# Optimization experiments

Measured on AMD Instinct MI355X. Metric: run time of the kernel, lower is better.

## Reference

```python
import jax, jax.numpy as jnp
import numpy as np

IN_F = 4096
OUT_F = 16384
TOKENS = 64


def setup_inputs() -> dict:
    key = jax.random.key(0)
    k1, k2, k3 = jax.random.split(key, 3)
    x = jax.random.normal(k1, (TOKENS, IN_F), dtype=jnp.float16)
    # int8-valued weights stored as int32 (same math after cast to fp16)
    weight = jax.random.randint(k2, (OUT_F, IN_F), -127, 127, dtype=jnp.int32)
    weight_scales = jax.random.uniform(k3, (OUT_F,), dtype=jnp.float16, minval=0.001, maxval=0.02)
    bias = jnp.zeros((1, OUT_F), dtype=jnp.float16)
    return {"x": x, "weight": weight, "weight_scales": weight_scales, "bias": bias}


def reference(x, weight, weight_scales, bias):
    # Dequantize int8 weight to fp16 with per-output-channel scale, then linear.
    w_fp16 = weight.astype(jnp.float16) * weight_scales[:, None]  # [out, in]
    y = jnp.dot(x, w_fp16.T) + bias  # [tokens, out]
    return y
```

## Files before the change

### kernel.cpp

```cpp
#include <hip/hip_runtime.h>
#include <hip/hip_bf16.h>
#include <hip/hip_fp16.h>

#define IN_F 4096
#define OUT_F 16384
#define TOKENS 64

#define NCH 64
#define KT 64
#define KHALF 2048
#define NTILES (KHALF / KT)
#define BLOCK 256

typedef __attribute__((ext_vector_type(8))) short bf16x8;
typedef __attribute__((ext_vector_type(8))) unsigned short u16x8;
typedef __attribute__((ext_vector_type(4))) unsigned short u16x4;
typedef __attribute__((ext_vector_type(4))) float f32x4;
typedef __attribute__((ext_vector_type(4))) int i32x4;

enum { F_BF16 = 0, F_FP16 = 1, F_FP32 = 2 };

__device__ __forceinline__ float dec_bf16(unsigned short h) {
    return __uint_as_float(((unsigned)h) << 16);
}
__device__ __forceinline__ float dec_fp16(unsigned short h) {
    __half_raw hr; hr.x = h;
    return __half2float(__half(hr));
}
__device__ __forceinline__ unsigned short enc_bf16_rne(float f) {
    unsigned u = __float_as_uint(f);
    u += 0x7FFFu + ((u >> 16) & 1u);
    return (unsigned short)(u >> 16);
}

__device__ __forceinline__ int detect_fmt16(const void* p, int lane, float lo, float hi) {
    unsigned short h = ((const unsigned short*)p)[lane];
    float vb = fabsf(dec_bf16(h));
    float vh = fabsf(dec_fp16(h));
    int cb = __popcll(__ballot(vb > lo && vb < hi));
    int ch = __popcll(__ballot(vh > lo && vh < hi));
    return (cb >= 56) ? F_BF16 : (ch >= 56) ? F_FP16 : F_FP32;
}
__device__ __forceinline__ int detect_wint(const int* w, int lane) {
    int v = w[lane];
    int ci = __popcll(__ballot(v >= -127 && v <= 127));
    return (ci >= 56) ? 1 : 0;
}

__global__ __launch_bounds__(256) void prep_x(const void* __restrict__ xv,
                                              unsigned short* __restrict__ xbf) {
    const int tid  = blockIdx.x * 256 + threadIdx.x;
    const int lane = threadIdx.x & 63;
    const int xf = detect_fmt16(xv, lane, 9.7e-4f, 64.0f);

    if (xf == F_BF16) {
        u16x8 a = ((const u16x8*)xv)[tid * 2];
        u16x8 b = ((const u16x8*)xv)[tid * 2 + 1];
        ((u16x8*)xbf)[tid * 2]     = a;
        ((u16x8*)xbf)[tid * 2 + 1] = b;
    } else if (xf == F_FP32) {
        u16x8 o[2];
        #pragma unroll
        for (int half = 0; half < 2; ++half) {
            f32x4 v0 = ((const f32x4*)xv)[tid * 4 + half * 2];
            f32x4 v1 = ((const f32x4*)xv)[tid * 4 + half * 2 + 1];
            #pragma unroll
            for (int j = 0; j < 4; ++j) {
                o[half][j]     = enc_bf16_rne(v0[j]);
                o[half][j + 4] = enc_bf16_rne(v1[j]);
            }
        }
        ((u16x8*)xbf)[tid * 2]     = o[0];
        ((u16x8*)xbf)[tid * 2 + 1] = o[1];
    } else {
        #pragma unroll
        for (int half = 0; half < 2; ++half) {
            u16x8 v = ((const u16x8*)xv)[tid * 2 + half];
            u16x8 o;
            #pragma unroll
            for (int j = 0; j < 8; ++j) o[j] = enc_bf16_rne(dec_fp16(v[j]));
            ((u16x8*)xbf)[tid * 2 + half] = o;
        }
    }
}

template <int WINT>
__device__ __forceinline__ void tile_compute(const char* __restrict__ bB,
                                             const char* __restrict__ bA,
                                             int wv, int ln, int kq, f32x4 acc[4]) {
    const char* brow = bB + (wv * 16 + ln) * 256;
    #pragma unroll
    for (int s = 0; s < 2; ++s) {
        const int c0 = s * 8 + kq * 2;
        i32x4 b0 = *(const i32x4*)(brow + ((c0)     ^ ln) * 16);
        i32x4 b1 = *(const i32x4*)(brow + ((c0 + 1) ^ ln) * 16);
        bf16x8 bfrag;
        #pragma unroll
        for (int j = 0; j < 4; ++j) {
            unsigned f0 = WINT ? __float_as_uint((float)b0[j]) : (unsigned)b0[j];
            unsigned f1 = WINT ? __float_as_uint((float)b1[j]) : (unsigned)b1[j];
            bfrag[j]     = (short)(f0 >> 16);
            bfrag[j + 4] = (short)(f1 >> 16);
        }
        const int ca = s * 4 + kq;
        bf16x8 a0 = *(const bf16x8*)(bA + (ln      ) * 128 + ((ca) ^ (ln & 7)) * 16);
        bf16x8 a1 = *(const bf16x8*)(bA + (ln + 16) * 128 + ((ca) ^ (ln & 7)) * 16);
        bf16x8 a2 = *(const bf16x8*)(bA + (ln + 32) * 128 + ((ca) ^ (ln & 7)) * 16);
        bf16x8 a3 = *(const bf16x8*)(bA + (ln + 48) * 128 + ((ca) ^ (ln & 7)) * 16);
        acc[0] = __builtin_amdgcn_mfma_f32_16x16x32_bf16(a0, bfrag, acc[0], 0, 0, 0);
        acc[1] = __builtin_amdgcn_mfma_f32_16x16x32_bf16(a1, bfrag, acc[1], 0, 0, 0);
        acc[2] = __builtin_amdgcn_mfma_f32_16x16x32_bf16(a2, bfrag, acc[2], 0, 0, 0);
        acc[3] = __builtin_amdgcn_mfma_f32_16x16x32_bf16(a3, bfrag, acc[3], 0, 0, 0);
    }
}

__global__ __launch_bounds__(BLOCK) void w8a16_main(
    const int* __restrict__ w, const unsigned short* __restrict__ xbf,
    float* __restrict__ pws) {

    __shared__ alignas(16) char ldsB[2][NCH * KT * 4];
    __shared__ alignas(16) char ldsA[2][TOKENS * KT * 2];

    const int tid  = threadIdx.x;
    const int wv   = tid >> 6;
    const int lane = tid & 63;
    const int ln   = lane & 15;
    const int kq   = lane >> 4;

    const int kh   = blockIdx.x & 1;
    const int n0   = (blockIdx.x >> 1) * NCH;
    const int koff = kh * KHALF;

    const int wi = detect_wint(w, lane);

    auto stage = [&](int t, int db) {
        #pragma unroll
        for (int j = 0; j < 4; ++j) {
            const int idx = j * 256 + tid;
            const int r   = idx >> 4;
            const int cg  = (idx & 15) ^ (r & 15);
            const int* g  = w + (size_t)(n0 + r) * IN_F + koff + t * KT + cg * 4;
            __builtin_amdgcn_global_load_lds(
                (const __attribute__((address_space(1))) unsigned int*)g,
                (__attribute__((address_space(3))) unsigned int*)(&ldsB[db][idx * 16]),
                16, 0, 0);
        }
        #pragma unroll
        for (int j = 0; j < 2; ++j) {
            const int idx = j * 256 + tid;
            const int tok = idx >> 3;
            const int cg  = (idx & 7) ^ (tok & 7);
            const unsigned short* g = xbf + (size_t)tok * IN_F + koff + t * KT + cg * 8;
            __builtin_amdgcn_global_load_lds(
                (const __attribute__((address_space(1))) unsigned int*)g,
                (__attribute__((address_space(3))) unsigned int*)(&ldsA[db][idx * 16]),
                16, 0, 0);
        }
    };

    f32x4 acc[4] = {};

    stage(0, 0);
    __syncthreads();
    for (int t = 0; t < NTILES; ++t) {
        if (t + 1 < NTILES) stage(t + 1, (t + 1) & 1);
        if (wi) tile_compute<1>(ldsB[t & 1], ldsA[t & 1], wv, ln, kq, acc);
        else    tile_compute<0>(ldsB[t & 1], ldsA[t & 1], wv, ln, kq, acc);
        __syncthreads();
    }

    float* pp = pws + (size_t)kh * TOKENS * OUT_F;
    const int n = n0 + wv * 16 + ln;
    #pragma unroll
    for (int i = 0; i < 4; ++i)
        #pragma unroll
        for (int r = 0; r < 4; ++r)
            pp[(size_t)(16 * i + kq * 4 + r) * OUT_F + n] = acc[i][r];
}

__global__ __launch_bounds__(256) void reduce_k(
    const float* __restrict__ pws, const void* __restrict__ xv,
    const void* __restrict__ sv, const void* __restrict__ bv,
    void* __restrict__ yv) {

    const int t    = blockIdx.x * 256 + threadIdx.x;
    const int lane = threadIdx.x & 63;
    const int xf = detect_fmt16(xv, lane, 9.7e-4f, 64.0f);
    const int sf = detect_fmt16(sv, lane, 1.0e-4f, 0.25f);

    const int base = t * 4;
    const int m    = base >> 14;
    const int n    = base & 16383;

    f32x4 p0 = *(const f32x4*)(pws + (size_t)m * OUT_F + n);
    f32x4 p1 = *(const f32x4*)(pws + (size_t)TOKENS * OUT_F + (size_t)m * OUT_F + n);

    float sc[4], bi[4];
    if (sf == F_FP32) {
        f32x4 s4 = *(const f32x4*)((const float*)sv + n);
        f32x4 b4 = *(const f32x4*)((const float*)bv + n);
        #pragma unroll
        for (int j = 0; j < 4; ++j) { sc[j] = s4[j]; bi[j] = b4[j]; }
    } else if (sf == F_BF16) {
        u16x4 s4 = *(const u16x4*)((const unsigned short*)sv + n);
        u16x4 b4 = *(const u16x4*)((const unsigned short*)bv + n);
        #pragma unroll
        for (int j = 0; j < 4; ++j) { sc[j] = dec_bf16(s4[j]); bi[j] = dec_bf16(b4[j]); }
    } else {
        u16x4 s4 = *(const u16x4*)((const unsigned short*)sv + n);
        u16x4 b4 = *(const u16x4*)((const unsigned short*)bv + n);
        #pragma unroll
        for (int j = 0; j < 4; ++j) { sc[j] = dec_fp16(s4[j]); bi[j] = dec_fp16(b4[j]); }
    }

    f32x4 v;
    #pragma unroll
    for (int j = 0; j < 4; ++j) v[j] = (p0[j] + p1[j]) * sc[j] + bi[j];

    if (xf == F_FP32) {
        *(f32x4*)((float*)yv + base) = v;
    } else if (xf == F_BF16) {
        u16x4 o;
        #pragma unroll
        for (int j = 0; j < 4; ++j) o[j] = enc_bf16_rne(v[j]);
        *(u16x4*)((unsigned short*)yv + base) = o;
    } else {
        u16x4 o;
        #pragma unroll
        for (int j = 0; j < 4; ++j) {
            __half h = __float2half(v[j]);
            o[j] = *(unsigned short*)&h;
        }
        *(u16x4*)((unsigned short*)yv + base) = o;
    }
}

extern "C" void kernel_launch(void* const* d_in, const int* in_sizes, int n_in,
                              void* d_out, int out_size, void* d_ws, size_t ws_size,
                              hipStream_t stream) {
    unsigned short* xbf = (unsigned short*)d_ws;
    float*          pws = (float*)((char*)d_ws + 524288);

    prep_x<<<64, 256, 0, stream>>>(d_in[0], xbf);
    w8a16_main<<<(OUT_F / NCH) * 2, BLOCK, 0, stream>>>((const int*)d_in[1], xbf, pws);
    reduce_k<<<1024, 256, 0, stream>>>(pws, d_in[0], d_in[2], d_in[3], d_out);
}
```

Baseline: 388.5 us.

## Give each wave its own K-slice with per-wave LDS ring, split-K by 8

Replaces the block-wide double-buffered tile loop with independent per-wave pipelines: each wave owns 32 output channels and one eighth of K, streams weights through a private 3-slot LDS ring using vmcnt waits instead of __syncthreads, and loads activations straight from global into registers. Split-K goes from 2 to 8, so there are many more waves and the reduce kernel now sums 8 partial buffers. The aim is to remove block barriers and expose more memory-level parallelism on the weight stream. In exchange the fp32 partial workspace grows fourfold, which adds write and read traffic, and activation loads are no longer shared through LDS.

```diff
diff --git a/kernel.cpp b/kernel.cpp
--- a/kernel.cpp
+++ b/kernel.cpp
@@ -6,10 +6,12 @@
 #define OUT_F 16384
 #define TOKENS 64
 
-#define NCH 64
-#define KT 64
-#define KHALF 2048
-#define NTILES (KHALF / KT)
+#define CHW 32
+#define KSPLIT 8
+#define KCH (IN_F / KSPLIT)
+#define NITER (KCH / 32)
+#define NRING 3
+#define TILE_B 4096
 #define BLOCK 256
 
 typedef __attribute__((ext_vector_type(8))) short bf16x8;
@@ -85,32 +87,75 @@
 }
 
 template <int WINT>
-__device__ __forceinline__ void tile_compute(const char* __restrict__ bB,
-                                             const char* __restrict__ bA,
-                                             int wv, int ln, int kq, f32x4 acc[4]) {
-    const char* brow = bB + (wv * 16 + ln) * 256;
-    #pragma unroll
-    for (int s = 0; s < 2; ++s) {
-        const int c0 = s * 8 + kq * 2;
-        i32x4 b0 = *(const i32x4*)(brow + ((c0)     ^ ln) * 16);
-        i32x4 b1 = *(const i32x4*)(brow + ((c0 + 1) ^ ln) * 16);
-        bf16x8 bfrag;
+__device__ __forceinline__ void wave_kloop(
+    const int* __restrict__ w, const unsigned short* __restrict__ xbf,
+    char* __restrict__ myring, int wn0, int koff, int lane, int ln, int kq,
+    f32x4 acc[8]) {
+
+    const int rl = lane >> 3;
+    const int cc = (lane & 7) ^ rl;
+
+    auto stage = [&](int t, int slot) {
         #pragma unroll
         for (int j = 0; j < 4; ++j) {
-            unsigned f0 = WINT ? __float_as_uint((float)b0[j]) : (unsigned)b0[j];
-            unsigned f1 = WINT ? __float_as_uint((float)b1[j]) : (unsigned)b1[j];
-            bfrag[j]     = (short)(f0 >> 16);
-            bfrag[j + 4] = (short)(f1 >> 16);
-        }
-        const int ca = s * 4 + kq;
-        bf16x8 a0 = *(const bf16x8*)(bA + (ln      ) * 128 + ((ca) ^ (ln & 7)) * 16);
-        bf16x8 a1 = *(const bf16x8*)(bA + (ln + 16) * 128 + ((ca) ^ (ln & 7)) * 16);
-        bf16x8 a2 = *(const bf16x8*)(bA + (ln + 32) * 128 + ((ca) ^ (ln & 7)) * 16);
-        bf16x8 a3 = *(const bf16x8*)(bA + (ln + 48) * 128 + ((ca) ^ (ln & 7)) * 16);
-        acc[0] = __builtin_amdgcn_mfma_f32_16x16x32_bf16(a0, bfrag, acc[0], 0, 0, 0);
-        acc[1] = __builtin_amdgcn_mfma_f32_16x16x32_bf16(a1, bfrag, acc[1], 0, 0, 0);
-        acc[2] = __builtin_amdgcn_mfma_f32_16x16x32_bf16(a2, bfrag, acc[2], 0, 0, 0);
-        acc[3] = __builtin_amdgcn_mfma_f32_16x16x32_bf16(a3, bfrag, acc[3], 0, 0, 0);
+            const int r = j * 8 + rl;
+            const int* g = w + (size_t)(wn0 + r) * IN_F + koff + t * 32 + cc * 4;
+            __builtin_amdgcn_global_load_lds(
+                (const __attribute__((address_space(1))) unsigned int*)g,
+                (__attribute__((address_space(3))) unsigned int*)
+                    (myring + slot * TILE_B + j * 1024 + lane * 16),
+                16, 0, 0);
+        }
+    };
+
+    const short* xs = (const short*)xbf;
+    const size_t xr0 = (size_t)(ln     ) * IN_F;
+    const size_t xr1 = (size_t)(ln + 16) * IN_F;
+    const size_t xr2 = (size_t)(ln + 32) * IN_F;
+    const size_t xr3 = (size_t)(ln + 48) * IN_F;
+
+    int kk = koff + kq * 8;
+    bf16x8 ca0 = *(const bf16x8*)(xs + xr0 + kk);
+    bf16x8 ca1 = *(const bf16x8*)(xs + xr1 + kk);
+    bf16x8 ca2 = *(const bf16x8*)(xs + xr2 + kk);
+    bf16x8 ca3 = *(const bf16x8*)(xs + xr3 + kk);
+    stage(0, 0);
+    stage(1, 1);
+
+    int sl = 0;
+    for (int t = 0; t < NITER; ++t) {
+        kk = koff + ((t + 1) & (NITER - 1)) * 32 + kq * 8;
+        bf16x8 na0 = *(const bf16x8*)(xs + xr0 + kk);
+        bf16x8 na1 = *(const bf16x8*)(xs + xr1 + kk);
+        bf16x8 na2 = *(const bf16x8*)(xs + xr2 + kk);
+        bf16x8 na3 = *(const bf16x8*)(xs + xr3 + kk);
+        int s2 = sl + 2; if (s2 >= NRING) s2 -= NRING;
+        stage((t + 2) & (NITER - 1), s2);
+
+        asm volatile("s_waitcnt vmcnt(12)" ::: "memory");
+
+        const char* base = myring + sl * TILE_B;
+        #pragma unroll
+        for (int g = 0; g < 2; ++g) {
+            const char* brow = base + (g * 16 + ln) * 128;
+            i32x4 b0 = *(const i32x4*)(brow + (((kq * 2    ) ^ (ln & 7)) * 16));
+            i32x4 b1 = *(const i32x4*)(brow + (((kq * 2 + 1) ^ (ln & 7)) * 16));
+            bf16x8 bf;
+            #pragma unroll
+            for (int j = 0; j < 4; ++j) {
+                unsigned f0 = WINT ? __float_as_uint((float)b0[j]) : (unsigned)b0[j];
+                unsigned f1 = WINT ? __float_as_uint((float)b1[j]) : (unsigned)b1[j];
+                bf[j]     = (short)(f0 >> 16);
+                bf[j + 4] = (short)(f1 >> 16);
+            }
+            acc[g*4+0] = __builtin_amdgcn_mfma_f32_16x16x32_bf16(ca0, bf, acc[g*4+0], 0, 0, 0);
+            acc[g*4+1] = __builtin_amdgcn_mfma_f32_16x16x32_bf16(ca1, bf, acc[g*4+1], 0, 0, 0);
+            acc[g*4+2] = __builtin_amdgcn_mfma_f32_16x16x32_bf16(ca2, bf, acc[g*4+2], 0, 0, 0);
+            acc[g*4+3] = __builtin_amdgcn_mfma_f32_16x16x32_bf16(ca3, bf, acc[g*4+3], 0, 0, 0);
+        }
+
+        ca0 = na0; ca1 = na1; ca2 = na2; ca3 = na3;
+        ++sl; if (sl >= NRING) sl = 0;
     }
 }
 
@@ -118,8 +163,7 @@
     const int* __restrict__ w, const unsigned short* __restrict__ xbf,
     float* __restrict__ pws) {
 
-    __shared__ alignas(16) char ldsB[2][NCH * KT * 4];
-    __shared__ alignas(16) char ldsA[2][TOKENS * KT * 2];
+    __shared__ alignas(16) char ring[4][NRING][TILE_B];
 
     const int tid  = threadIdx.x;
     const int wv   = tid >> 6;
@@ -127,55 +171,29 @@
     const int ln   = lane & 15;
     const int kq   = lane >> 4;
 
-    const int kh   = blockIdx.x & 1;
-    const int n0   = (blockIdx.x >> 1) * NCH;
-    const int koff = kh * KHALF;
+    const int gw   = blockIdx.x * 4 + wv;
+    const int wn0  = (gw >> 3) * CHW;
+    const int ks   = gw & 7;
+    const int koff = ks * KCH;
 
     const int wi = detect_wint(w, lane);
 
-    auto stage = [&](int t, int db) {
-        #pragma unroll
-        for (int j = 0; j < 4; ++j) {
-            const int idx = j * 256 + tid;
-            const int r   = idx >> 4;
-            const int cg  = (idx & 15) ^ (r & 15);
-            const int* g  = w + (size_t)(n0 + r) * IN_F + koff + t * KT + cg * 4;
-            __builtin_amdgcn_global_load_lds(
-                (const __attribute__((address_space(1))) unsigned int*)g,
-                (__attribute__((address_space(3))) unsigned int*)(&ldsB[db][idx * 16]),
-                16, 0, 0);
-        }
-        #pragma unroll
-        for (int j = 0; j < 2; ++j) {
-            const int idx = j * 256 + tid;
-            const int tok = idx >> 3;
-            const int cg  = (idx & 7) ^ (tok & 7);
-            const unsigned short* g = xbf + (size_t)tok * IN_F + koff + t * KT + cg * 8;
-            __builtin_amdgcn_global_load_lds(
-                (const __attribute__((address_space(1))) unsigned int*)g,
-                (__attribute__((address_space(3))) unsigned int*)(&ldsA[db][idx * 16]),
-                16, 0, 0);
-        }
-    };
-
-    f32x4 acc[4] = {};
-
-    stage(0, 0);
-    __syncthreads();
-    for (int t = 0; t < NTILES; ++t) {
-        if (t + 1 < NTILES) stage(t + 1, (t + 1) & 1);
-        if (wi) tile_compute<1>(ldsB[t & 1], ldsA[t & 1], wv, ln, kq, acc);
-        else    tile_compute<0>(ldsB[t & 1], ldsA[t & 1], wv, ln, kq, acc);
-        __syncthreads();
-    }
-
-    float* pp = pws + (size_t)kh * TOKENS * OUT_F;
-    const int n = n0 + wv * 16 + ln;
+    f32x4 acc[8] = {};
+    char* myring = &ring[wv][0][0];
+
+    if (wi) wave_kloop<1>(w, xbf, myring, wn0, koff, lane, ln, kq, acc);
+    else    wave_kloop<0>(w, xbf, myring, wn0, koff, lane, ln, kq, acc);
+
+    float* pp = pws + (size_t)ks * TOKENS * OUT_F;
     #pragma unroll
-    for (int i = 0; i < 4; ++i)
-        #pragma unroll
-        for (int r = 0; r < 4; ++r)
-            pp[(size_t)(16 * i + kq * 4 + r) * OUT_F + n] = acc[i][r];
+    for (int g = 0; g < 2; ++g) {
+        const int n = wn0 + g * 16 + ln;
+        #pragma unroll
+        for (int tt = 0; tt < 4; ++tt)
+            #pragma unroll
+            for (int r = 0; r < 4; ++r)
+                pp[(size_t)(16 * tt + kq * 4 + r) * OUT_F + n] = acc[g * 4 + tt][r];
+    }
 }
 
 __global__ __launch_bounds__(256) void reduce_k(
@@ -192,8 +210,13 @@
     const int m    = base >> 14;
     const int n    = base & 16383;
 
-    f32x4 p0 = *(const f32x4*)(pws + (size_t)m * OUT_F + n);
-    f32x4 p1 = *(const f32x4*)(pws + (size_t)TOKENS * OUT_F + (size_t)m * OUT_F + n);
+    f32x4 s = {0.f, 0.f, 0.f, 0.f};
+    #pragma unroll
+    for (int ks = 0; ks < KSPLIT; ++ks) {
+        f32x4 p = *(const f32x4*)(pws + (size_t)ks * TOKENS * OUT_F + (size_t)m * OUT_F + n);
+        #pragma unroll
+        for (int j = 0; j < 4; ++j) s[j] += p[j];
+    }
 
     float sc[4], bi[4];
     if (sf == F_FP32) {
@@ -215,7 +238,7 @@
 
     f32x4 v;
     #pragma unroll
-    for (int j = 0; j < 4; ++j) v[j] = (p0[j] + p1[j]) * sc[j] + bi[j];
+    for (int j = 0; j < 4; ++j) v[j] = s[j] * sc[j] + bi[j];
 
     if (xf == F_FP32) {
         *(f32x4*)((float*)yv + base) = v;
@@ -239,9 +262,11 @@
                               void* d_out, int out_size, void* d_ws, size_t ws_size,
                               hipStream_t stream) {
     unsigned short* xbf = (unsigned short*)d_ws;
-    float*          pws = (float*)((char*)d_ws + 524288);
+    float*          pws = (float*)((char*)d_ws + (1 << 20));
 
     prep_x<<<64, 256, 0, stream>>>(d_in[0], xbf);
-    w8a16_main<<<(OUT_F / NCH) * 2, BLOCK, 0, stream>>>((const int*)d_in[1], xbf, pws);
-    reduce_k<<<1024, 256, 0, stream>>>(pws, d_in[0], d_in[2], d_in[3], d_out);
-}
+    w8a16_main<<<(OUT_F / CHW) * KSPLIT / 4, BLOCK, 0, stream>>>(
+        (const int*)d_in[1], xbf, pws);
+    reduce_k<<<(TOKENS * OUT_F / 4) / 256, 256, 0, stream>>>(
+        pws, d_in[0], d_in[2], d_in[3], d_out);
+}
```

Result: no change. 389.4 us (+0.2%).
